# Kernel optimization log

Hardware: AMD Instinct MI355X
Metric: run time of the kernel (lower is better)

The kernel has to match this reference:

```python
import jax, jax.numpy as jnp
import numpy as np

N_NODES = 100000
N_EDGES = 600000
N_CLASS = 26
HIDDEN = 128


def setup_inputs() -> dict:
    key = jax.random.key(0)
    ks = jax.random.split(key, 8)
    x = jax.random.normal(ks[0], (N_NODES, N_CLASS), dtype=jnp.float32)
    edge_index = jax.random.randint(ks[1], (2, N_EDGES), 0, N_NODES, dtype=jnp.int64)
    edge_weight = jax.random.uniform(ks[2], (N_EDGES,), dtype=jnp.float32)
    W1 = jax.random.normal(ks[3], (N_CLASS, HIDDEN), dtype=jnp.float32) * (1.0 / np.sqrt(N_CLASS))
    b1 = jnp.zeros((HIDDEN,), dtype=jnp.float32)
    W2 = jax.random.normal(ks[4], (HIDDEN, HIDDEN), dtype=jnp.float32) * (1.0 / np.sqrt(HIDDEN))
    b2 = jnp.zeros((HIDDEN,), dtype=jnp.float32)
    Wfc = jax.random.normal(ks[5], (HIDDEN, N_CLASS), dtype=jnp.float32) * (1.0 / np.sqrt(HIDDEN))
    bfc = jnp.zeros((N_CLASS,), dtype=jnp.float32)
    return {"x": x, "edge_index": edge_index, "edge_weight": edge_weight,
            "W1": W1, "b1": b1, "W2": W2, "b2": b2, "Wfc": Wfc, "bfc": bfc}


def _gcn_norm(edge_index, edge_weight, n_nodes):
    # PyG gcn_norm: add self-loops (weight 1), symmetric deg^-1/2 normalization.
    loop = jnp.arange(n_nodes, dtype=edge_index.dtype)
    row = jnp.concatenate([edge_index[0], loop])  # source
    col = jnp.concatenate([edge_index[1], loop])  # destination
    w = jnp.concatenate([edge_weight, jnp.ones((n_nodes,), edge_weight.dtype)])
    deg = jax.ops.segment_sum(w, col, num_segments=n_nodes)
    d_inv_sqrt = jnp.where(deg > 0, jax.lax.rsqrt(jnp.maximum(deg, 1e-12)), 0.0)
    norm = d_inv_sqrt[row] * w * d_inv_sqrt[col]
    return row, col, norm


def _gcn_conv(x, row, col, norm, W, b, n_nodes):
    h = x @ W                              # [N, out]
    msg = norm[:, None] * h[row]           # gather + scale, [E+N, out]
    out = jax.ops.segment_sum(msg, col, num_segments=n_nodes)  # scatter-add
    return out + b


def reference(x, edge_index, edge_weight, W1, b1, W2, b2, Wfc, bfc):
    n = x.shape[0]
    row, col, norm = _gcn_norm(edge_index, edge_weight, n)
    h = jax.nn.relu(_gcn_conv(x, row, col, norm, W1, b1, n))
    h = jax.nn.relu(_gcn_conv(h, row, col, norm, W2, b2, n))
    return h @ Wfc + bfc
```

## Files before the change

### kernel.cpp

```cpp
#include <hip/hip_runtime.h>

#define NNODES 100000
#define NEDGES 600000
#define NCLASS 26
#define HID    128

#define SHIFT  9
#define BCOLS  512
#define NBKT   196
#define EPB    1024
#define NBE    586
#define NH     (NBKT * NBE)

typedef __attribute__((ext_vector_type(8))) _Float16 f16x8;
typedef __attribute__((ext_vector_type(4))) float f32x4;

__device__ inline unsigned short f2h(float f) {
    union { _Float16 h; unsigned short s; } c;
    c.h = (_Float16)f;
    return c.s;
}
__device__ inline unsigned int packh(float a, float b) {
    return (unsigned int)f2h(a) | ((unsigned int)f2h(b) << 16);
}
__device__ inline float hlo(unsigned int p) {
    union { unsigned short s; _Float16 h; } c;
    c.s = (unsigned short)p;
    return (float)c.h;
}
__device__ inline float hhi(unsigned int p) {
    union { unsigned short s; _Float16 h; } c;
    c.s = (unsigned short)(p >> 16);
    return (float)c.h;
}

__device__ inline void fma16(float* acc, float v, uint4 g0, uint4 g1) {
    acc[0]  = fmaf(v, hlo(g0.x), acc[0]);  acc[1]  = fmaf(v, hhi(g0.x), acc[1]);
    acc[2]  = fmaf(v, hlo(g0.y), acc[2]);  acc[3]  = fmaf(v, hhi(g0.y), acc[3]);
    acc[4]  = fmaf(v, hlo(g0.z), acc[4]);  acc[5]  = fmaf(v, hhi(g0.z), acc[5]);
    acc[6]  = fmaf(v, hlo(g0.w), acc[6]);  acc[7]  = fmaf(v, hhi(g0.w), acc[7]);
    acc[8]  = fmaf(v, hlo(g1.x), acc[8]);  acc[9]  = fmaf(v, hhi(g1.x), acc[9]);
    acc[10] = fmaf(v, hlo(g1.y), acc[10]); acc[11] = fmaf(v, hhi(g1.y), acc[11]);
    acc[12] = fmaf(v, hlo(g1.z), acc[12]); acc[13] = fmaf(v, hhi(g1.z), acc[13]);
    acc[14] = fmaf(v, hlo(g1.w), acc[14]); acc[15] = fmaf(v, hhi(g1.w), acc[15]);
}

__global__ __launch_bounds__(256) void histA_k(const int* __restrict__ col,
                                               int* __restrict__ H) {
    __shared__ int h[NBKT];
    int t = threadIdx.x;
    for (int i = t; i < NBKT; i += 256) h[i] = 0;
    __syncthreads();
    int base = blockIdx.x * EPB;
#pragma unroll
    for (int u = 0; u < 4; u++) {
        int e = base + t + u * 256;
        if (e < NEDGES) atomicAdd(&h[col[e] >> SHIFT], 1);
    }
    __syncthreads();
    for (int i = t; i < NBKT; i += 256) H[i * NBE + blockIdx.x] = h[i];
}

__global__ void scanH1_k(const int* __restrict__ in, int* __restrict__ incl,
                         int* __restrict__ aux, int n) {
    __shared__ int s[256];
    int t = threadIdx.x, gi = blockIdx.x * 256 + t;
    s[t] = (gi < n) ? in[gi] : 0;
    __syncthreads();
    for (int off = 1; off < 256; off <<= 1) {
        int x = (t >= off) ? s[t - off] : 0;
        __syncthreads();
        s[t] += x;
        __syncthreads();
    }
    if (gi < n) incl[gi] = s[t];
    if (t == 255) aux[blockIdx.x] = s[255];
}

__global__ void scan2_k(int* __restrict__ aux, int n) {
    __shared__ int s[512];
    int t = threadIdx.x;
    s[t] = (t < n) ? aux[t] : 0;
    __syncthreads();
    for (int off = 1; off < 512; off <<= 1) {
        int x = (t >= off) ? s[t - off] : 0;
        __syncthreads();
        s[t] += x;
        __syncthreads();
    }
    if (t < n) aux[t] = s[t];
}

__device__ inline int exoff(const int* __restrict__ incl, const int* __restrict__ H,
                            const int* __restrict__ aux, int gi) {
    int add = (gi >= 256) ? aux[(gi >> 8) - 1] : 0;
    return incl[gi] - H[gi] + add;
}

__global__ __launch_bounds__(256) void partB_k(const int* __restrict__ row,
                                               const int* __restrict__ col,
                                               const float* __restrict__ w,
                                               const int* __restrict__ incl,
                                               const int* __restrict__ H,
                                               const int* __restrict__ aux,
                                               uint2* __restrict__ rw,
                                               unsigned short* __restrict__ lc) {
    __shared__ int off[NBKT];
    __shared__ int cur[NBKT];
    int t = threadIdx.x;
    for (int i = t; i < NBKT; i += 256) {
        off[i] = exoff(incl, H, aux, i * NBE + blockIdx.x);
        cur[i] = 0;
    }
    __syncthreads();
    int base = blockIdx.x * EPB;
#pragma unroll
    for (int u = 0; u < 4; u++) {
        int e = base + t + u * 256;
        if (e < NEDGES) {
            int c = col[e], b = c >> SHIFT;
            int p = off[b] + atomicAdd(&cur[b], 1);
            rw[p] = make_uint2((unsigned int)row[e], __float_as_uint(w[e]));
            lc[p] = (unsigned short)(c & (BCOLS - 1));
        }
    }
}

__global__ __launch_bounds__(256) void segbp_k(const uint2* __restrict__ rw,
                                               const unsigned short* __restrict__ lc,
                                               const int* __restrict__ incl,
                                               const int* __restrict__ H,
                                               const int* __restrict__ aux,
                                               int* __restrict__ rowptr,
                                               float* __restrict__ dis,
                                               uint2* __restrict__ meta) {
    __shared__ int   cnt[BCOLS];
    __shared__ float ws[BCOLS];
    __shared__ int   rpl[BCOLS];
    __shared__ int   ps[256];
    int b = blockIdx.x, t = threadIdx.x;
    int c0 = b << SHIFT;
    int ncols = min(BCOLS, NNODES - c0);
    for (int i = t; i < BCOLS; i += 256) { cnt[i] = 0; ws[i] = 0.f; }
    __syncthreads();
    int s    = exoff(incl, H, aux, b * NBE);
    int eend = (b == NBKT - 1) ? NEDGES : exoff(incl, H, aux, (b + 1) * NBE);
    for (int e = s + t; e < eend; e += 256) {
        uint2 m = rw[e];
        int l = lc[e];
        atomicAdd(&cnt[l], 1);
        atomicAdd(&ws[l], __uint_as_float(m.y));
    }
    __syncthreads();
    for (int i = t; i < ncols; i += 256) dis[c0 + i] = rsqrtf(1.0f + ws[i]);
    int a0 = cnt[2 * t], a1 = cnt[2 * t + 1];
    ps[t] = a0 + a1;
    __syncthreads();
    for (int off = 1; off < 256; off <<= 1) {
        int x = (t >= off) ? ps[t - off] : 0;
        __syncthreads();
        ps[t] += x;
        __syncthreads();
    }
    int ex = (t > 0) ? ps[t - 1] : 0;
    rpl[2 * t]     = s + ex;
    rpl[2 * t + 1] = s + ex + a0;
    if (2 * t     < ncols) rowptr[c0 + 2 * t]     = s + ex;
    if (2 * t + 1 < ncols) rowptr[c0 + 2 * t + 1] = s + ex + a0;
    if (b == NBKT - 1 && t == 0) rowptr[NNODES] = NEDGES;
    cnt[2 * t] = 0; cnt[2 * t + 1] = 0;
    __syncthreads();
    for (int e = s + t; e < eend; e += 256) {
        uint2 m = rw[e];
        int l = lc[e];
        int pos = rpl[l] + atomicAdd(&cnt[l], 1);
        meta[pos] = make_uint2(m.x, m.y);
    }
}

__global__ __launch_bounds__(256) void prep_k(const float* __restrict__ W2,
                                              const float* __restrict__ W1,
                                              const float* __restrict__ Wfc,
                                              const float* __restrict__ x,
                                              const float* __restrict__ dis,
                                              unsigned short* __restrict__ wt,
                                              unsigned short* __restrict__ w1t,
                                              unsigned short* __restrict__ wfct,
                                              unsigned int* __restrict__ xp) {
    int b = blockIdx.x, t = threadIdx.x;
    if (b < 64) {
        int idx = b * 256 + t;
        int c = idx >> 7, k = idx & 127;
        wt[c * 128 + k] = f2h(W2[k * 128 + c]);
    } else if (b < 80) {
        int idx = (b - 64) * 256 + t;
        int c = idx >> 5, k = idx & 31;
        w1t[c * 32 + k] = (k < NCLASS) ? f2h(W1[k * 128 + c]) : (unsigned short)0;
    } else if (b < 96) {
        int idx = (b - 80) * 256 + t;
        int c = idx >> 7, k = idx & 127;
        wfct[c * 128 + k] = (c < NCLASS) ? f2h(Wfc[k * NCLASS + c]) : (unsigned short)0;
    } else {
        int i = (b - 96) * 256 + t;
        if (i < NNODES * 16) {
            int r = i >> 4, u = i & 15, f0 = u * 2;
            float d = dis[r];
            float a = (f0     < NCLASS) ? x[r * NCLASS + f0]     : 0.f;
            float c = (f0 + 1 < NCLASS) ? x[r * NCLASS + f0 + 1] : 0.f;
            xp[i] = packh(d * a, d * c);
        }
    }
}

__global__ __launch_bounds__(256) void agg26_k(const int* __restrict__ rowptr,
                                               const uint2* __restrict__ meta,
                                               const unsigned int* __restrict__ xp,
                                               const float* __restrict__ dis,
                                               unsigned int* __restrict__ aggx) {
    int node = blockIdx.x * 32 + (threadIdx.x >> 3);
    int l8 = threadIdx.x & 7;
    const uint2* xp2 = (const uint2*)xp;

    uint2 self = xp2[(size_t)node * 8 + l8];
    float acc[4] = { hlo(self.x), hhi(self.x), hlo(self.y), hhi(self.y) };
    int j = rowptr[node], jend = rowptr[node + 1];
    for (; j < jend; j++) {
        uint2 m = meta[j];
        uint2 g = xp2[(size_t)m.x * 8 + l8];
        float v = __uint_as_float(m.y);
        acc[0] = fmaf(v, hlo(g.x), acc[0]); acc[1] = fmaf(v, hhi(g.x), acc[1]);
        acc[2] = fmaf(v, hlo(g.y), acc[2]); acc[3] = fmaf(v, hhi(g.y), acc[3]);
    }
    float d = dis[node];
    ((uint2*)aggx)[(size_t)node * 8 + l8] =
        make_uint2(packh(d * acc[0], d * acc[1]), packh(d * acc[2], d * acc[3]));
}

__global__ __launch_bounds__(256) void gemm12_k(const unsigned short* __restrict__ aggx,
                                                const unsigned short* __restrict__ w1t,
                                                const float* __restrict__ b1,
                                                const unsigned short* __restrict__ wt,
                                                const float* __restrict__ dis,
                                                unsigned short* __restrict__ C, int N) {
    __shared__ unsigned short h1s[64 * 136];
    __shared__ unsigned short Ws[128 * 72];
    const int tid  = threadIdx.x;
    const int wv = tid >> 6, lane = tid & 63;
    const int quad = lane >> 4, l16 = lane & 15;
    const int row0 = blockIdx.x * 64;
    const int wrow = wv * 16;

#pragma unroll
    for (int jj = 0; jj < 4; jj++) {
        int idx = tid + jj * 256;
        int r = idx >> 3, ku = idx & 7;
        *(uint4*)&Ws[r * 72 + ku * 8] = *(const uint4*)&wt[(size_t)r * 128 + ku * 8];
    }

    {
        int ar = row0 + wrow + l16;
        f16x8 af1 = (ar < N) ? *(const f16x8*)&aggx[(size_t)ar * 32 + quad * 8]
                             : (f16x8)(_Float16)0.f;
#pragma unroll
        for (int n = 0; n < 8; n++) {
            f16x8 bw = *(const f16x8*)&w1t[(n * 16 + l16) * 32 + quad * 8];
            f32x4 hacc = __builtin_amdgcn_mfma_f32_16x16x32_f16(af1, bw, (f32x4)0.f, 0, 0, 0);
            int col = n * 16 + l16;
            float bv = b1[col];
#pragma unroll
            for (int r = 0; r < 4; r++)
                h1s[(wrow + quad * 4 + r) * 136 + col] = f2h(fmaxf(hacc[r] + bv, 0.f));
        }
    }
    __syncthreads();

    f16x8 af[4];
#pragma unroll
    for (int kc = 0; kc < 4; kc++)
        af[kc] = *(const f16x8*)&h1s[(wrow + l16) * 136 + kc * 32 + quad * 8];

    f32x4 acc[8];
#pragma unroll
    for (int n = 0; n < 8; n++) acc[n] = (f32x4)0.f;

    for (int c = 0; c < 2; c++) {
        if (c == 1) {
            __syncthreads();
#pragma unroll
            for (int jj = 0; jj < 4; jj++) {
                int idx = tid + jj * 256;
                int r = idx >> 3, ku = idx & 7;
                *(uint4*)&Ws[r * 72 + ku * 8] =
                    *(const uint4*)&wt[(size_t)r * 128 + 64 + ku * 8];
            }
            __syncthreads();
        }
#pragma unroll
        for (int n = 0; n < 8; n++) {
#pragma unroll
            for (int kc = 0; kc < 2; kc++) {
                f16x8 bfr = *(const f16x8*)&Ws[(n * 16 + l16) * 72 + kc * 32 + quad * 8];
                acc[n] = __builtin_amdgcn_mfma_f32_16x16x32_f16(
                    af[c * 2 + kc], bfr, acc[n], 0, 0, 0);
            }
        }
    }

    const int rbase = row0 + wrow + quad * 4;
    float dv[4];
#pragma unroll
    for (int r = 0; r < 4; r++)
        dv[r] = (rbase + r < N) ? dis[rbase + r] : 0.f;
#pragma unroll
    for (int n = 0; n < 8; n++) {
        int col = n * 16 + l16;
#pragma unroll
        for (int r = 0; r < 4; r++) {
            if (rbase + r < N)
                C[(size_t)(rbase + r) * 128 + col] = f2h(dv[r] * acc[n][r]);
        }
    }
}

__global__ __launch_bounds__(256) void aggfc_k(const int* __restrict__ rowptr,
                                               const uint2* __restrict__ meta,
                                               const uint4* __restrict__ h4,
                                               const float* __restrict__ dis,
                                               const float* __restrict__ b2,
                                               const unsigned short* __restrict__ wfct,
                                               const float* __restrict__ bfc,
                                               float* __restrict__ out, int N) {
    __shared__ unsigned short h2s[64 * 136];
    const int tid = threadIdx.x;
    const int wv = tid >> 6, lane = tid & 63;
    const int grp = lane >> 3, l8 = lane & 7;
    const int nbase = blockIdx.x * 64;

    for (int p = 0; p < 2; p++) {
        int r = wv * 16 + p * 8 + grp;
        int node = nbase + r;
        float acc[16];
        float d = 0.f;
        if (node < N) {
            d = dis[node];
            uint4 s0 = h4[(size_t)node * 16 + l8 * 2];
            uint4 s1 = h4[(size_t)node * 16 + l8 * 2 + 1];
            acc[0]  = hlo(s0.x); acc[1]  = hhi(s0.x);
            acc[2]  = hlo(s0.y); acc[3]  = hhi(s0.y);
            acc[4]  = hlo(s0.z); acc[5]  = hhi(s0.z);
            acc[6]  = hlo(s0.w); acc[7]  = hhi(s0.w);
            acc[8]  = hlo(s1.x); acc[9]  = hhi(s1.x);
            acc[10] = hlo(s1.y); acc[11] = hhi(s1.y);
            acc[12] = hlo(s1.z); acc[13] = hhi(s1.z);
            acc[14] = hlo(s1.w); acc[15] = hhi(s1.w);
            int j = rowptr[node], jend = rowptr[node + 1];
            for (; j < jend; j++) {
                uint2 m = meta[j];
                uint4 g0 = h4[(size_t)m.x * 16 + l8 * 2];
                uint4 g1 = h4[(size_t)m.x * 16 + l8 * 2 + 1];
                fma16(acc, __uint_as_float(m.y), g0, g1);
            }
        } else {
#pragma unroll
            for (int k = 0; k < 16; k++) acc[k] = 0.f;
        }
        unsigned int wpk[8];
#pragma unroll
        for (int q = 0; q < 4; q++) {
            float4 bv = ((const float4*)b2)[l8 * 4 + q];
            float a0 = fmaxf(fmaf(d, acc[q * 4 + 0], bv.x), 0.f);
            float a1 = fmaxf(fmaf(d, acc[q * 4 + 1], bv.y), 0.f);
            float a2 = fmaxf(fmaf(d, acc[q * 4 + 2], bv.z), 0.f);
            float a3 = fmaxf(fmaf(d, acc[q * 4 + 3], bv.w), 0.f);
            if (node >= N) { a0 = a1 = a2 = a3 = 0.f; }
            wpk[q * 2]     = packh(a0, a1);
            wpk[q * 2 + 1] = packh(a2, a3);
        }
        *(uint4*)&h2s[r * 136 + l8 * 16] =
            make_uint4(wpk[0], wpk[1], wpk[2], wpk[3]);
        *(uint4*)&h2s[r * 136 + l8 * 16 + 8] =
            make_uint4(wpk[4], wpk[5], wpk[6], wpk[7]);
    }

    const int q = lane >> 4, m = lane & 15;
    f16x8 af[4];
#pragma unroll
    for (int ks = 0; ks < 4; ks++)
        af[ks] = *(const f16x8*)&h2s[(wv * 16 + m) * 136 + ks * 32 + q * 8];

#pragma unroll
    for (int n = 0; n < 2; n++) {
        f32x4 o = (f32x4)0.f;
#pragma unroll
        for (int ks = 0; ks < 4; ks++) {
            f16x8 bfr = *(const f16x8*)&wfct[(size_t)(n * 16 + m) * 128 + ks * 32 + q * 8];
            o = __builtin_amdgcn_mfma_f32_16x16x32_f16(af[ks], bfr, o, 0, 0, 0);
        }
        int col = n * 16 + m;
        if (col < NCLASS) {
            float bv = bfc[col];
            int r0 = nbase + wv * 16 + q * 4;
#pragma unroll
            for (int r = 0; r < 4; r++) {
                if (r0 + r < N)
                    out[(size_t)(r0 + r) * NCLASS + col] = o[r] + bv;
            }
        }
    }
}

extern "C" void kernel_launch(void* const* d_in, const int* in_sizes, int n_in,
                              void* d_out, int out_size, void* d_ws, size_t ws_size,
                              hipStream_t stream) {
    const float* x   = (const float*)d_in[0];
    const int*   ei  = (const int*)d_in[1];
    const float* ew  = (const float*)d_in[2];
    const float* W1  = (const float*)d_in[3];
    const float* b1  = (const float*)d_in[4];
    const float* W2  = (const float*)d_in[5];
    const float* b2  = (const float*)d_in[6];
    const float* Wfc = (const float*)d_in[7];
    const float* bfc = (const float*)d_in[8];
    float* out = (float*)d_out;

    const int N = NNODES;
    const int* erow = ei;
    const int* ecol = ei + NEDGES;

    float* fws    = (float*)d_ws;
    float* dis    = fws;
    int*   rowptr = (int*)(fws + 100000);
    int*   H      = (int*)(fws + 200004);
    int*   incl   = (int*)(fws + 314860);
    int*   aux    = (int*)(fws + 429716);
    uint2* rw     = (uint2*)(fws + 430228);
    unsigned short* lc = (unsigned short*)(fws + 1630228);
    uint2* meta   = (uint2*)(fws + 1930228);
    unsigned short* wt16   = (unsigned short*)(fws + 3130228);
    unsigned short* w1t16  = (unsigned short*)(fws + 3138420);
    unsigned short* wfct16 = (unsigned short*)(fws + 3140468);
    unsigned int*   xp     = (unsigned int*)(fws + 3142516);
    unsigned int*   aggx   = (unsigned int*)(fws + 4742516);
    unsigned short* hB16   = (unsigned short*)(fws + 6342516);

    const int gScan = (NH + 255) / 256;
    const int gA26  = N / 32;
    const int gPrep = 96 + (N * 16 + 255) / 256;
    const int g64   = (N + 63) / 64;

    histA_k<<<NBE, 256, 0, stream>>>(ecol, H);
    scanH1_k<<<gScan, 256, 0, stream>>>(H, incl, aux, NH);
    scan2_k<<<1, 512, 0, stream>>>(aux, gScan);
    partB_k<<<NBE, 256, 0, stream>>>(erow, ecol, ew, incl, H, aux, rw, lc);
    segbp_k<<<NBKT, 256, 0, stream>>>(rw, lc, incl, H, aux, rowptr, dis, meta);

    prep_k<<<gPrep, 256, 0, stream>>>(W2, W1, Wfc, x, dis, wt16, w1t16, wfct16, xp);

    agg26_k<<<gA26, 256, 0, stream>>>(rowptr, meta, xp, dis, aggx);
    gemm12_k<<<g64, 256, 0, stream>>>((const unsigned short*)aggx, w1t16, b1,
                                      wt16, dis, hB16, N);

    aggfc_k<<<g64, 256, 0, stream>>>(rowptr, meta, (const uint4*)hB16, dis, b2,
                                     wfct16, bfc, out, N);
}
```

Before: 201.0 us.

## Replace histogram-scan partition with atomic bucket slots and fuse layer-1 aggregation into GEMM

Drops the per-block histogram, the two-level scan and the separate partition pass. Each block now reserves space in fixed-capacity bucket slots through a global atomic counter, and the true bucket offsets are computed by a small scan inside the segment kernel. The first-layer 26-wide aggregation is also merged into the GEMM kernel, so the intermediate aggx buffer is no longer written and read back, and the kernel count drops. In exchange, correctness depends on no bucket holding more than BSLOT edges, which random inputs are expected to satisfy, and the order of edges within a bucket now depends on the order of atomic updates.

Result: no change. 204.3 us (+1.7%).

```diff
diff --git a/kernel.cpp b/kernel.cpp
--- a/kernel.cpp
+++ b/kernel.cpp
@@ -10,7 +10,7 @@
 #define NBKT   196
 #define EPB    1024
 #define NBE    586
-#define NH     (NBKT * NBE)
+#define BSLOT  4096
 
 typedef __attribute__((ext_vector_type(8))) _Float16 f16x8;
 typedef __attribute__((ext_vector_type(4))) float f32x4;
@@ -45,114 +45,83 @@
     acc[14] = fmaf(v, hlo(g1.w), acc[14]); acc[15] = fmaf(v, hhi(g1.w), acc[15]);
 }
 
-__global__ __launch_bounds__(256) void histA_k(const int* __restrict__ col,
-                                               int* __restrict__ H) {
-    __shared__ int h[NBKT];
+__global__ __launch_bounds__(256) void initc_k(int* __restrict__ gcur) {
     int t = threadIdx.x;
-    for (int i = t; i < NBKT; i += 256) h[i] = 0;
-    __syncthreads();
-    int base = blockIdx.x * EPB;
-#pragma unroll
-    for (int u = 0; u < 4; u++) {
-        int e = base + t + u * 256;
-        if (e < NEDGES) atomicAdd(&h[col[e] >> SHIFT], 1);
-    }
-    __syncthreads();
-    for (int i = t; i < NBKT; i += 256) H[i * NBE + blockIdx.x] = h[i];
-}
-
-__global__ void scanH1_k(const int* __restrict__ in, int* __restrict__ incl,
-                         int* __restrict__ aux, int n) {
-    __shared__ int s[256];
-    int t = threadIdx.x, gi = blockIdx.x * 256 + t;
-    s[t] = (gi < n) ? in[gi] : 0;
-    __syncthreads();
-    for (int off = 1; off < 256; off <<= 1) {
-        int x = (t >= off) ? s[t - off] : 0;
-        __syncthreads();
-        s[t] += x;
-        __syncthreads();
-    }
-    if (gi < n) incl[gi] = s[t];
-    if (t == 255) aux[blockIdx.x] = s[255];
-}
-
-__global__ void scan2_k(int* __restrict__ aux, int n) {
-    __shared__ int s[512];
-    int t = threadIdx.x;
-    s[t] = (t < n) ? aux[t] : 0;
-    __syncthreads();
-    for (int off = 1; off < 512; off <<= 1) {
-        int x = (t >= off) ? s[t - off] : 0;
-        __syncthreads();
-        s[t] += x;
-        __syncthreads();
-    }
-    if (t < n) aux[t] = s[t];
-}
-
-__device__ inline int exoff(const int* __restrict__ incl, const int* __restrict__ H,
-                            const int* __restrict__ aux, int gi) {
-    int add = (gi >= 256) ? aux[(gi >> 8) - 1] : 0;
-    return incl[gi] - H[gi] + add;
-}
-
-__global__ __launch_bounds__(256) void partB_k(const int* __restrict__ row,
+    if (t < NBKT) gcur[t] = 0;
+}
+
+__global__ __launch_bounds__(256) void partC_k(const int* __restrict__ row,
                                                const int* __restrict__ col,
                                                const float* __restrict__ w,
-                                               const int* __restrict__ incl,
-                                               const int* __restrict__ H,
-                                               const int* __restrict__ aux,
+                                               int* __restrict__ gcur,
                                                uint2* __restrict__ rw,
                                                unsigned short* __restrict__ lc) {
+    __shared__ int h[NBKT];
     __shared__ int off[NBKT];
     __shared__ int cur[NBKT];
     int t = threadIdx.x;
-    for (int i = t; i < NBKT; i += 256) {
-        off[i] = exoff(incl, H, aux, i * NBE + blockIdx.x);
-        cur[i] = 0;
-    }
+    for (int i = t; i < NBKT; i += 256) { h[i] = 0; cur[i] = 0; }
     __syncthreads();
     int base = blockIdx.x * EPB;
+    int cc[4]; int rr[4]; float ww[4];
 #pragma unroll
     for (int u = 0; u < 4; u++) {
         int e = base + t + u * 256;
         if (e < NEDGES) {
-            int c = col[e], b = c >> SHIFT;
+            cc[u] = col[e]; rr[u] = row[e]; ww[u] = w[e];
+            atomicAdd(&h[cc[u] >> SHIFT], 1);
+        } else cc[u] = -1;
+    }
+    __syncthreads();
+    for (int i = t; i < NBKT; i += 256)
+        off[i] = i * BSLOT + atomicAdd(&gcur[i], h[i]);
+    __syncthreads();
+#pragma unroll
+    for (int u = 0; u < 4; u++) {
+        if (cc[u] >= 0) {
+            int b = cc[u] >> SHIFT;
             int p = off[b] + atomicAdd(&cur[b], 1);
-            rw[p] = make_uint2((unsigned int)row[e], __float_as_uint(w[e]));
-            lc[p] = (unsigned short)(c & (BCOLS - 1));
-        }
-    }
-}
-
-__global__ __launch_bounds__(256) void segbp_k(const uint2* __restrict__ rw,
-                                               const unsigned short* __restrict__ lc,
-                                               const int* __restrict__ incl,
-                                               const int* __restrict__ H,
-                                               const int* __restrict__ aux,
-                                               int* __restrict__ rowptr,
-                                               float* __restrict__ dis,
-                                               uint2* __restrict__ meta) {
+            rw[p] = make_uint2((unsigned int)rr[u], __float_as_uint(ww[u]));
+            lc[p] = (unsigned short)(cc[u] & (BCOLS - 1));
+        }
+    }
+}
+
+__global__ __launch_bounds__(256) void segbp2_k(const uint2* __restrict__ rw,
+                                                const unsigned short* __restrict__ lc,
+                                                const int* __restrict__ gcur,
+                                                int* __restrict__ rowptr,
+                                                float* __restrict__ dis,
+                                                uint2* __restrict__ meta) {
     __shared__ int   cnt[BCOLS];
-    __shared__ float ws[BCOLS];
+    __shared__ float wsum[BCOLS];
     __shared__ int   rpl[BCOLS];
     __shared__ int   ps[256];
+    __shared__ int   bs[256];
     int b = blockIdx.x, t = threadIdx.x;
+    bs[t] = (t < NBKT) ? gcur[t] : 0;
+    __syncthreads();
+    for (int off = 1; off < 256; off <<= 1) {
+        int x = (t >= off) ? bs[t - off] : 0;
+        __syncthreads();
+        bs[t] += x;
+        __syncthreads();
+    }
+    int nb    = gcur[b];
+    int strue = bs[b] - nb;
+    int sloc  = b * BSLOT;
     int c0 = b << SHIFT;
     int ncols = min(BCOLS, NNODES - c0);
-    for (int i = t; i < BCOLS; i += 256) { cnt[i] = 0; ws[i] = 0.f; }
-    __syncthreads();
-    int s    = exoff(incl, H, aux, b * NBE);
-    int eend = (b == NBKT - 1) ? NEDGES : exoff(incl, H, aux, (b + 1) * NBE);
-    for (int e = s + t; e < eend; e += 256) {
+    for (int i = t; i < BCOLS; i += 256) { cnt[i] = 0; wsum[i] = 0.f; }
+    __syncthreads();
+    for (int e = sloc + t; e < sloc + nb; e += 256) {
         uint2 m = rw[e];
         int l = lc[e];
         atomicAdd(&cnt[l], 1);
-        atomicAdd(&ws[l], __uint_as_float(m.y));
-    }
-    __syncthreads();
-    for (int i = t; i < ncols; i += 256) dis[c0 + i] = rsqrtf(1.0f + ws[i]);
+        atomicAdd(&wsum[l], __uint_as_float(m.y));
+    }
+    __syncthreads();
+    for (int i = t; i < ncols; i += 256) dis[c0 + i] = rsqrtf(1.0f + wsum[i]);
     int a0 = cnt[2 * t], a1 = cnt[2 * t + 1];
     ps[t] = a0 + a1;
     __syncthreads();
@@ -163,14 +132,14 @@
         __syncthreads();
     }
     int ex = (t > 0) ? ps[t - 1] : 0;
-    rpl[2 * t]     = s + ex;
-    rpl[2 * t + 1] = s + ex + a0;
-    if (2 * t     < ncols) rowptr[c0 + 2 * t]     = s + ex;
-    if (2 * t + 1 < ncols) rowptr[c0 + 2 * t + 1] = s + ex + a0;
+    rpl[2 * t]     = strue + ex;
+    rpl[2 * t + 1] = strue + ex + a0;
+    if (2 * t     < ncols) rowptr[c0 + 2 * t]     = strue + ex;
+    if (2 * t + 1 < ncols) rowptr[c0 + 2 * t + 1] = strue + ex + a0;
     if (b == NBKT - 1 && t == 0) rowptr[NNODES] = NEDGES;
     cnt[2 * t] = 0; cnt[2 * t + 1] = 0;
     __syncthreads();
-    for (int e = s + t; e < eend; e += 256) {
+    for (int e = sloc + t; e < sloc + nb; e += 256) {
         uint2 m = rw[e];
         int l = lc[e];
         int pos = rpl[l] + atomicAdd(&cnt[l], 1);
@@ -212,36 +181,14 @@
     }
 }
 
-__global__ __launch_bounds__(256) void agg26_k(const int* __restrict__ rowptr,
-                                               const uint2* __restrict__ meta,
-                                               const unsigned int* __restrict__ xp,
-                                               const float* __restrict__ dis,
-                                               unsigned int* __restrict__ aggx) {
-    int node = blockIdx.x * 32 + (threadIdx.x >> 3);
-    int l8 = threadIdx.x & 7;
-    const uint2* xp2 = (const uint2*)xp;
-
-    uint2 self = xp2[(size_t)node * 8 + l8];
-    float acc[4] = { hlo(self.x), hhi(self.x), hlo(self.y), hhi(self.y) };
-    int j = rowptr[node], jend = rowptr[node + 1];
-    for (; j < jend; j++) {
-        uint2 m = meta[j];
-        uint2 g = xp2[(size_t)m.x * 8 + l8];
-        float v = __uint_as_float(m.y);
-        acc[0] = fmaf(v, hlo(g.x), acc[0]); acc[1] = fmaf(v, hhi(g.x), acc[1]);
-        acc[2] = fmaf(v, hlo(g.y), acc[2]); acc[3] = fmaf(v, hhi(g.y), acc[3]);
-    }
-    float d = dis[node];
-    ((uint2*)aggx)[(size_t)node * 8 + l8] =
-        make_uint2(packh(d * acc[0], d * acc[1]), packh(d * acc[2], d * acc[3]));
-}
-
-__global__ __launch_bounds__(256) void gemm12_k(const unsigned short* __restrict__ aggx,
-                                                const unsigned short* __restrict__ w1t,
-                                                const float* __restrict__ b1,
-                                                const unsigned short* __restrict__ wt,
-                                                const float* __restrict__ dis,
-                                                unsigned short* __restrict__ C, int N) {
+__global__ __launch_bounds__(256) void agggemm_k(const int* __restrict__ rowptr,
+                                                 const uint2* __restrict__ meta,
+                                                 const uint4* __restrict__ xp4,
+                                                 const unsigned short* __restrict__ w1t,
+                                                 const float* __restrict__ b1,
+                                                 const unsigned short* __restrict__ wt,
+                                                 const float* __restrict__ dis,
+                                                 unsigned short* __restrict__ C, int N) {
     __shared__ unsigned short h1s[64 * 136];
     __shared__ unsigned short Ws[128 * 72];
     const int tid  = threadIdx.x;
@@ -257,20 +204,43 @@
         *(uint4*)&Ws[r * 72 + ku * 8] = *(const uint4*)&wt[(size_t)r * 128 + ku * 8];
     }
 
+    f16x8 af1;
     {
         int ar = row0 + wrow + l16;
-        f16x8 af1 = (ar < N) ? *(const f16x8*)&aggx[(size_t)ar * 32 + quad * 8]
-                             : (f16x8)(_Float16)0.f;
-#pragma unroll
-        for (int n = 0; n < 8; n++) {
-            f16x8 bw = *(const f16x8*)&w1t[(n * 16 + l16) * 32 + quad * 8];
-            f32x4 hacc = __builtin_amdgcn_mfma_f32_16x16x32_f16(af1, bw, (f32x4)0.f, 0, 0, 0);
-            int col = n * 16 + l16;
-            float bv = b1[col];
-#pragma unroll
-            for (int r = 0; r < 4; r++)
-                h1s[(wrow + quad * 4 + r) * 136 + col] = f2h(fmaxf(hacc[r] + bv, 0.f));
-        }
+        if (ar < N) {
+            float acc[8];
+            uint4 s = xp4[(size_t)ar * 4 + quad];
+            acc[0] = hlo(s.x); acc[1] = hhi(s.x);
+            acc[2] = hlo(s.y); acc[3] = hhi(s.y);
+            acc[4] = hlo(s.z); acc[5] = hhi(s.z);
+            acc[6] = hlo(s.w); acc[7] = hhi(s.w);
+            int j = rowptr[ar], jend = rowptr[ar + 1];
+            for (; j < jend; j++) {
+                uint2 m = meta[j];
+                uint4 g = xp4[(size_t)m.x * 4 + quad];
+                float v = __uint_as_float(m.y);
+                acc[0] = fmaf(v, hlo(g.x), acc[0]); acc[1] = fmaf(v, hhi(g.x), acc[1]);
+                acc[2] = fmaf(v, hlo(g.y), acc[2]); acc[3] = fmaf(v, hhi(g.y), acc[3]);
+                acc[4] = fmaf(v, hlo(g.z), acc[4]); acc[5] = fmaf(v, hhi(g.z), acc[5]);
+                acc[6] = fmaf(v, hlo(g.w), acc[6]); acc[7] = fmaf(v, hhi(g.w), acc[7]);
+            }
+            float d = dis[ar];
+#pragma unroll
+            for (int k = 0; k < 8; k++) af1[k] = (_Float16)(d * acc[k]);
+        } else {
+            af1 = (f16x8)(_Float16)0.f;
+        }
+    }
+
+#pragma unroll
+    for (int n = 0; n < 8; n++) {
+        f16x8 bw = *(const f16x8*)&w1t[(n * 16 + l16) * 32 + quad * 8];
+        f32x4 hacc = __builtin_amdgcn_mfma_f32_16x16x32_f16(af1, bw, (f32x4)0.f, 0, 0, 0);
+        int col = n * 16 + l16;
+        float bv = b1[col];
+#pragma unroll
+        for (int r = 0; r < 4; r++)
+            h1s[(wrow + quad * 4 + r) * 136 + col] = f2h(fmaxf(hacc[r] + bv, 0.f));
     }
     __syncthreads();
 
@@ -279,9 +249,9 @@
     for (int kc = 0; kc < 4; kc++)
         af[kc] = *(const f16x8*)&h1s[(wrow + l16) * 136 + kc * 32 + quad * 8];
 
-    f32x4 acc[8];
-#pragma unroll
-    for (int n = 0; n < 8; n++) acc[n] = (f32x4)0.f;
+    f32x4 acc2[8];
+#pragma unroll
+    for (int n = 0; n < 8; n++) acc2[n] = (f32x4)0.f;
 
     for (int c = 0; c < 2; c++) {
         if (c == 1) {
@@ -300,8 +270,8 @@
 #pragma unroll
             for (int kc = 0; kc < 2; kc++) {
                 f16x8 bfr = *(const f16x8*)&Ws[(n * 16 + l16) * 72 + kc * 32 + quad * 8];
-                acc[n] = __builtin_amdgcn_mfma_f32_16x16x32_f16(
-                    af[c * 2 + kc], bfr, acc[n], 0, 0, 0);
+                acc2[n] = __builtin_amdgcn_mfma_f32_16x16x32_f16(
+                    af[c * 2 + kc], bfr, acc2[n], 0, 0, 0);
             }
         }
     }
@@ -317,7 +287,7 @@
 #pragma unroll
         for (int r = 0; r < 4; r++) {
             if (rbase + r < N)
-                C[(size_t)(rbase + r) * 128 + col] = f2h(dv[r] * acc[n][r]);
+                C[(size_t)(rbase + r) * 128 + col] = f2h(dv[r] * acc2[n][r]);
         }
     }
 }
@@ -430,35 +400,27 @@
     float* fws    = (float*)d_ws;
     float* dis    = fws;
     int*   rowptr = (int*)(fws + 100000);
-    int*   H      = (int*)(fws + 200004);
-    int*   incl   = (int*)(fws + 314860);
-    int*   aux    = (int*)(fws + 429716);
-    uint2* rw     = (uint2*)(fws + 430228);
-    unsigned short* lc = (unsigned short*)(fws + 1630228);
-    uint2* meta   = (uint2*)(fws + 1930228);
-    unsigned short* wt16   = (unsigned short*)(fws + 3130228);
-    unsigned short* w1t16  = (unsigned short*)(fws + 3138420);
-    unsigned short* wfct16 = (unsigned short*)(fws + 3140468);
-    unsigned int*   xp     = (unsigned int*)(fws + 3142516);
-    unsigned int*   aggx   = (unsigned int*)(fws + 4742516);
-    unsigned short* hB16   = (unsigned short*)(fws + 6342516);
-
-    const int gScan = (NH + 255) / 256;
-    const int gA26  = N / 32;
+    int*   gcur   = (int*)(fws + 200004);
+    uint2* rw     = (uint2*)(fws + 200204);
+    unsigned short* lc = (unsigned short*)(fws + 1805836);
+    uint2* meta   = (uint2*)(fws + 2207244);
+    unsigned short* wt16   = (unsigned short*)(fws + 3407244);
+    unsigned short* w1t16  = (unsigned short*)(fws + 3415436);
+    unsigned short* wfct16 = (unsigned short*)(fws + 3417484);
+    unsigned int*   xp     = (unsigned int*)(fws + 3419532);
+    unsigned short* hB16   = (unsigned short*)(fws + 5019532);
+
     const int gPrep = 96 + (N * 16 + 255) / 256;
     const int g64   = (N + 63) / 64;
 
-    histA_k<<<NBE, 256, 0, stream>>>(ecol, H);
-    scanH1_k<<<gScan, 256, 0, stream>>>(H, incl, aux, NH);
-    scan2_k<<<1, 512, 0, stream>>>(aux, gScan);
-    partB_k<<<NBE, 256, 0, stream>>>(erow, ecol, ew, incl, H, aux, rw, lc);
-    segbp_k<<<NBKT, 256, 0, stream>>>(rw, lc, incl, H, aux, rowptr, dis, meta);
+    initc_k<<<1, 256, 0, stream>>>(gcur);
+    partC_k<<<NBE, 256, 0, stream>>>(erow, ecol, ew, gcur, rw, lc);
+    segbp2_k<<<NBKT, 256, 0, stream>>>(rw, lc, gcur, rowptr, dis, meta);
 
     prep_k<<<gPrep, 256, 0, stream>>>(W2, W1, Wfc, x, dis, wt16, w1t16, wfct16, xp);
 
-    agg26_k<<<gA26, 256, 0, stream>>>(rowptr, meta, xp, dis, aggx);
-    gemm12_k<<<g64, 256, 0, stream>>>((const unsigned short*)aggx, w1t16, b1,
-                                      wt16, dis, hB16, N);
+    agggemm_k<<<g64, 256, 0, stream>>>(rowptr, meta, (const uint4*)xp, w1t16, b1,
+                                       wt16, dis, hB16, N);
 
     aggfc_k<<<g64, 256, 0, stream>>>(rowptr, meta, (const uint4*)hB16, dis, b2,
                                      wfct16, bfc, out, N);
```
